# Kernel optimization log

Measured on AMD Instinct MI355X. Metric: run time of the kernel, lower is better.

The kernel has to match this reference:

```python
import jax, jax.numpy as jnp
from jax import lax
import numpy as np

B, C, H, W = 32, 128, 32, 32
ZDIM = 256
KH = KW = 3
NB_UNITS = C * C * KH * KW  # 147456
BN_EPS = 1e-6


def setup_inputs() -> dict:
    key = jax.random.key(0)
    ks = jax.random.split(key, 5)
    x = jax.random.normal(ks[0], (B, C, H, W), dtype=jnp.float32)
    z = jax.random.normal(ks[1], (B, ZDIM), dtype=jnp.float32)
    # glorot-uniform Dense kernel
    limit = np.sqrt(6.0 / (ZDIM + NB_UNITS)).astype(np.float32)
    dense_w = jax.random.uniform(ks[2], (ZDIM, NB_UNITS), dtype=jnp.float32,
                                 minval=-limit, maxval=limit)
    dense_b = jnp.zeros((NB_UNITS,), dtype=jnp.float32)
    # gamma initialized to +/- 0.02 (scale_for_weights)
    sign = jnp.where(jax.random.bernoulli(ks[3], 0.5, (NB_UNITS,)), 1.0, -1.0)
    gamma = (0.02 * sign).astype(jnp.float32)
    beta = jnp.zeros((NB_UNITS,), dtype=jnp.float32)
    b = jnp.zeros((C,), dtype=jnp.float32)  # deconv bias (zeros in original)
    return {"x": x, "z": z, "dense_w": dense_w, "dense_b": dense_b,
            "gamma": gamma, "beta": beta, "b": b}


def _per_sample_deconv(xi, wi):
    # xi: (C,H,W); wi: (C_in=stack, C_out=filter, KH, KW)
    # out[f,p,q] = sum_{s,u,v} xi[s, p+u-1, q+v-1] * wi[s,f,u,v]
    k = jnp.transpose(wi, (1, 0, 2, 3))  # OIHW: (f, s, u, v)
    y = lax.conv_general_dilated(xi[None], k, window_strides=(1, 1),
                                 padding=[(1, 1), (1, 1)],
                                 dimension_numbers=("NCHW", "OIHW", "NCHW"))
    return y[0]


def reference(x, z, dense_w, dense_b, gamma, beta, b):
    # hypernetwork: Dense(relu) -> BatchNorm(axis=1, batch stats) -> Reshape
    h = jax.nn.relu(z @ dense_w + dense_b)            # (B, NB_UNITS)
    mean = jnp.mean(h, axis=0)
    std = jnp.sqrt(jnp.var(h, axis=0))
    h = (h - mean) / (std + BN_EPS)
    h = gamma * h + beta
    Wk = h.reshape(B, C, C, KH, KW)                   # per-sample kernels (s,f,u,v)
    out = jax.vmap(_per_sample_deconv)(x, Wk)         # (B, C, H, W)
    out = out + b[None, :, None, None]
    return out + x                                    # residual add
```

## Files before the change

### kernel.cpp

```cpp
#include <hip/hip_runtime.h>

#define NB 147456
#define ZD 256
#define BSZ 32
#define CCH 128

typedef __attribute__((ext_vector_type(8))) short short8;
typedef __attribute__((ext_vector_type(16))) float floatx16;

__device__ __forceinline__ unsigned short f2bf(float f) {
    unsigned int u = __float_as_uint(f);
    return (unsigned short)((u + 0x7fffu + ((u >> 16) & 1u)) >> 16);
}
__device__ __forceinline__ unsigned pk(unsigned hi, unsigned lo) {
    return __builtin_amdgcn_perm(hi, lo, 0x07060302u);
}

__global__ __launch_bounds__(64, 4) void hyper_mfma(
    const float* __restrict__ z, const float* __restrict__ dw,
    const float* __restrict__ db, const float* __restrict__ gamma,
    const float* __restrict__ beta, unsigned short* __restrict__ wkn)
{
    int lane = threadIdx.x;
    int L = lane & 31;
    int klane = lane >> 5;
    int n0 = blockIdx.x * 64 + 2 * L;

    const float* zp  = z + L * 256 + klane * 8;
    const float* dwp = dw + (size_t)(klane * 8) * NB + n0;

    floatx16 acc[2];
#pragma unroll
    for (int t = 0; t < 2; t++)
#pragma unroll
        for (int r = 0; r < 16; r++) acc[t][r] = 0.f;

    float4 za[2], zb[2];
    unsigned ba[8][2], bb[8][2];
#define LOADZ(BUF, S)                                                         \
    { BUF[0] = *(const float4*)(zp + (S) * 16);                               \
      BUF[1] = *(const float4*)(zp + (S) * 16 + 4); }
#define LOADB(BUF, S)                                                         \
    _Pragma("unroll") for (int j = 0; j < 8; j++)                             \
        *(uint2*)&BUF[j][0] = *(const uint2*)(dwp + (size_t)((S) * 16 + j) * NB);
#define DOMFMA(ZBUF, BUF, S)                                                  \
    {                                                                         \
        uint4 au;                                                             \
        au.x = pk(__float_as_uint(ZBUF[0].y), __float_as_uint(ZBUF[0].x));    \
        au.y = pk(__float_as_uint(ZBUF[0].w), __float_as_uint(ZBUF[0].z));    \
        au.z = pk(__float_as_uint(ZBUF[1].y), __float_as_uint(ZBUF[1].x));    \
        au.w = pk(__float_as_uint(ZBUF[1].w), __float_as_uint(ZBUF[1].z));    \
        short8 af = *(short8*)&au;                                            \
        _Pragma("unroll") for (int t = 0; t < 2; t++) {                       \
            uint4 u;                                                          \
            u.x = pk(BUF[1][t], BUF[0][t]); u.y = pk(BUF[3][t], BUF[2][t]);   \
            u.z = pk(BUF[5][t], BUF[4][t]); u.w = pk(BUF[7][t], BUF[6][t]);   \
            acc[t] = __builtin_amdgcn_mfma_f32_32x32x16_bf16(                 \
                af, *(short8*)&u, acc[t], 0, 0, 0);                           \
        }                                                                     \
    }
    LOADZ(za, 0)
    LOADB(ba, 0)
#pragma unroll
    for (int s = 0; s < 16; s += 2) {
        LOADZ(zb, s + 1)
        LOADB(bb, s + 1)
        DOMFMA(za, ba, s)
        if (s + 2 < 16) { LOADZ(za, s + 2) LOADB(ba, s + 2) }
        DOMFMA(zb, bb, s + 1)
    }
#undef LOADZ
#undef LOADB
#undef DOMFMA

    float2 bias = *(const float2*)(db + n0);
    float2 gmm  = *(const float2*)(gamma + n0);
    float2 btt  = *(const float2*)(beta + n0);
    float bias_a[2] = { bias.x, bias.y };
    float gm_a[2]   = { gmm.x, gmm.y };
    float bt_a[2]   = { btt.x, btt.y };

    float sc_a[2], mn_a[2];
#pragma unroll
    for (int t = 0; t < 2; t++) {
        float sp = 0.f, qp = 0.f;
#pragma unroll
        for (int r = 0; r < 16; r++) {
            float v = fmaxf(acc[t][r] + bias_a[t], 0.f);
            acc[t][r] = v;
            sp += v; qp += v * v;
        }
        sp += __shfl_xor(sp, 32, 64);
        qp += __shfl_xor(qp, 32, 64);
        float mn = sp * (1.f / 32.f);
        float var = fmaxf(qp * (1.f / 32.f) - mn * mn, 0.f);
        mn_a[t] = mn;
        sc_a[t] = gm_a[t] / (sqrtf(var) + 1e-6f);
    }

#pragma unroll
    for (int r = 0; r < 16; r++) {
        int brow = (r & 3) + 8 * (r >> 2) + 4 * klane;
        float w0 = sc_a[0] * (acc[0][r] - mn_a[0]) + bt_a[0];
        float w1 = sc_a[1] * (acc[1][r] - mn_a[1]) + bt_a[1];
        unsigned o = (unsigned)f2bf(w0) | ((unsigned)f2bf(w1) << 16);
        *(unsigned*)&wkn[(size_t)brow * NB + n0] = o;
    }
}

__global__ __launch_bounds__(256) void repack_xt(
    const unsigned short* __restrict__ wkn, unsigned short* __restrict__ wkt,
    const float* __restrict__ x, unsigned short* __restrict__ xb16)
{
    __shared__ char lmem[16 * 580 * 4];
    int t = threadIdx.x;
    if (blockIdx.x < 256) {
        unsigned int* lt = (unsigned int*)lmem;
        int b = blockIdx.x >> 3;
        int s0 = (blockIdx.x & 7) * 16;
        const unsigned int* src = (const unsigned int*)wkn + ((size_t)b * NB >> 1) + (size_t)s0 * 576;
#pragma unroll
        for (int i = 0; i < 36; i++) {
            int idx = t + i * 256;
            int si = idx / 576;
            int j2 = idx - si * 576;
            lt[si * 580 + j2] = src[(size_t)si * 576 + j2];
        }
        __syncthreads();
        const unsigned short* ls = (const unsigned short*)lt;
#pragma unroll
        for (int i = 0; i < 9; i++) {
            int tau = t + i * 256;
            int f = tau & 127;
            int half = (tau >> 7) & 1;
            int uv = tau >> 8;
            int col = f * 9 + uv;
            unsigned short v[8];
#pragma unroll
            for (int ss = 0; ss < 8; ss++)
                v[ss] = ls[(half * 8 + ss) * 1160 + col];
            uint4 o;
            o.x = v[0] | ((unsigned)v[1] << 16);
            o.y = v[2] | ((unsigned)v[3] << 16);
            o.z = v[4] | ((unsigned)v[5] << 16);
            o.w = v[6] | ((unsigned)v[7] << 16);
            ((uint4*)wkt)[((((size_t)b * 9 + uv) * 16) + (s0 >> 3) + half) * 128 + f] = o;
        }
    } else {
        unsigned short* lx = (unsigned short*)lmem;
        int idx = blockIdx.x - 256;
        int p = idx & 31;
        int b = idx >> 5;
        const float* xp = x + (size_t)b * CCH * 1024 + p * 32;
#pragma unroll
        for (int i = 0; i < 16; i++) {
            int ii = t + i * 256;
            int s = ii >> 5;
            int q = ii & 31;
            lx[q * 130 + s] = f2bf(xp[(size_t)s * 1024 + q]);
        }
        __syncthreads();
#pragma unroll
        for (int i = 0; i < 2; i++) {
            int tau = t + i * 256;
            int q = tau & 31;
            int ch = tau >> 5;
            const unsigned short* r = &lx[q * 130 + ch * 8];
            uint4 o;
            o.x = r[0] | ((unsigned)r[1] << 16);
            o.y = r[2] | ((unsigned)r[3] << 16);
            o.z = r[4] | ((unsigned)r[5] << 16);
            o.w = r[6] | ((unsigned)r[7] << 16);
            ((uint4*)xb16)[(((size_t)b * 32 + p) * 16 + ch) * 32 + q] = o;
        }
    }
}

__global__ __launch_bounds__(256, 4) void conv_mfma(
    const float* __restrict__ x, const unsigned short* __restrict__ xb16,
    const unsigned short* __restrict__ wkt, const float* __restrict__ cb,
    float* __restrict__ out)
{
    __shared__ short8 lds8[3 * 16 * 34];
    int t = threadIdx.x;
    int w = blockIdx.x;
    int xcd = w & 7, slot = w >> 3;
    int b = (xcd << 2) | (slot & 3);
    int p0 = slot >> 2;
    int wid = t >> 6, lane = t & 63;
    int fbase = wid * 32;
    int qcol = lane & 31, klane = lane >> 5;

    if (t < 96) {
        int r = t >> 5;
        int ch = (t >> 1) & 15;
        int col = (t & 1) * 33;
        short8 zz = { 0, 0, 0, 0, 0, 0, 0, 0 };
        lds8[(r * 16 + ch) * 34 + col] = zz;
    }
    const uint4* xsrc = (const uint4*)xb16;
#pragma unroll
    for (int i = 0; i < 6; i++) {
        int tau = t + i * 256;
        int q = tau & 31;
        int ch = (tau >> 5) & 15;
        int r = tau >> 9;
        int prow = p0 - 1 + r;
        uint4 v = make_uint4(0, 0, 0, 0);
        if (prow >= 0 && prow < 32)
            v = xsrc[(((size_t)b * 32 + prow) * 16 + ch) * 32 + q];
        *(uint4*)&lds8[(r * 16 + ch) * 34 + q + 1] = v;
    }
    __syncthreads();

    floatx16 acc;
#pragma unroll
    for (int r = 0; r < 16; r++) acc[r] = 0.f;

    const short8* A8 = (const short8*)wkt + ((size_t)b * 9 << 11);
    short8 Abuf0[3], Abuf1[3];

#define LOAD3(BUF, ST)                                                        \
    {                                                                         \
        int v_ = (ST) >> 3, ks_ = (ST) & 7;                                   \
        int ko_ = ks_ * 2 + klane;                                            \
        _Pragma("unroll") for (int u_ = 0; u_ < 3; u_++)                      \
            BUF[u_] = A8[(((size_t)(u_ * 3 + v_) * 16 + ko_) << 7) + fbase + qcol]; \
    }
#define COMPUTE(BUF, ST)                                                      \
    {                                                                         \
        int v_ = (ST) >> 3, ks_ = (ST) & 7;                                   \
        int ko_ = ks_ * 2 + klane;                                            \
        short8 br[3];                                                         \
        _Pragma("unroll") for (int u_ = 0; u_ < 3; u_++)                      \
            br[u_] = lds8[(u_ * 16 + ko_) * 34 + qcol + v_];                  \
        _Pragma("unroll") for (int u_ = 0; u_ < 3; u_++)                      \
            acc = __builtin_amdgcn_mfma_f32_32x32x16_bf16(                    \
                BUF[u_], br[u_], acc, 0, 0, 0);                               \
    }

    LOAD3(Abuf0, 0)
    for (int st = 0; st < 24; st += 2) {
        LOAD3(Abuf1, st + 1)
        COMPUTE(Abuf0, st)
        if (st + 2 < 24) LOAD3(Abuf0, st + 2)
        COMPUTE(Abuf1, st + 1)
    }
#undef LOAD3
#undef COMPUTE

    const size_t xb = (size_t)b * CCH * 1024;
#pragma unroll
    for (int r = 0; r < 16; r++) {
        int fl = (r & 3) + 8 * (r >> 2) + 4 * klane;
        int f = fbase + fl;
        size_t idx = xb + (size_t)f * 1024 + p0 * 32 + qcol;
        out[idx] = acc[r] + x[idx] + cb[f];
    }
}

extern "C" void kernel_launch(void* const* d_in, const int* in_sizes, int n_in,
                              void* d_out, int out_size, void* d_ws, size_t ws_size,
                              hipStream_t stream) {
    const float* x     = (const float*)d_in[0];
    const float* z     = (const float*)d_in[1];
    const float* dw    = (const float*)d_in[2];
    const float* db    = (const float*)d_in[3];
    const float* gamma = (const float*)d_in[4];
    const float* beta  = (const float*)d_in[5];
    const float* cb    = (const float*)d_in[6];
    float* out = (float*)d_out;

    unsigned short* wkn  = (unsigned short*)d_ws;
    unsigned short* wkt  = (unsigned short*)((char*)d_ws + (size_t)BSZ * NB * 2);
    unsigned short* xb16 = (unsigned short*)((char*)d_ws + (size_t)BSZ * NB * 4);

    hyper_mfma<<<NB / 64, 64, 0, stream>>>(z, dw, db, gamma, beta, wkn);
    repack_xt<<<256 + 1024, 256, 0, stream>>>(wkn, wkt, x, xb16);
    conv_mfma<<<1024, 256, 0, stream>>>(x, xb16, wkt, cb, out);
}
```

Baseline: 262.0 us.

## Move x bf16 repack into hypernet kernel and triple-buffer conv weight loads

The x-to-bf16 transpose blocks move out of the weight repack kernel and are appended as extra 64-thread blocks of the hypernetwork kernel, so they run alongside the dense GEMM instead of in the repack launch. The repack kernel becomes weight-only. Separately, the conv kernel's A-operand prefetch goes from double to triple buffering with a fully unrolled loop, to hide more global-load latency. The extra blocks add LDS to every hyper_mfma block, and the third buffer adds registers, which may lower occupancy.

```diff
diff --git a/kernel.cpp b/kernel.cpp
--- a/kernel.cpp
+++ b/kernel.cpp
@@ -19,9 +19,41 @@
 __global__ __launch_bounds__(64, 4) void hyper_mfma(
     const float* __restrict__ z, const float* __restrict__ dw,
     const float* __restrict__ db, const float* __restrict__ gamma,
-    const float* __restrict__ beta, unsigned short* __restrict__ wkn)
+    const float* __restrict__ beta, unsigned short* __restrict__ wkn,
+    const float* __restrict__ x, unsigned short* __restrict__ xb16)
 {
+    __shared__ unsigned short lx[32 * 130];
     int lane = threadIdx.x;
+
+    if (blockIdx.x >= 2304) {
+        int idx = blockIdx.x - 2304;
+        int p = idx & 31;
+        int b = idx >> 5;
+        const float* xp = x + (size_t)b * CCH * 1024 + p * 32;
+#pragma unroll 8
+        for (int i = 0; i < 64; i++) {
+            int ii = lane + i * 64;
+            int s = ii >> 5;
+            int q = ii & 31;
+            lx[q * 130 + s] = f2bf(xp[(size_t)s * 1024 + q]);
+        }
+        __syncthreads();
+#pragma unroll
+        for (int i = 0; i < 8; i++) {
+            int tau = lane + i * 64;
+            int q = tau & 31;
+            int ch = tau >> 5;
+            const unsigned short* r = &lx[q * 130 + ch * 8];
+            uint4 o;
+            o.x = r[0] | ((unsigned)r[1] << 16);
+            o.y = r[2] | ((unsigned)r[3] << 16);
+            o.z = r[4] | ((unsigned)r[5] << 16);
+            o.w = r[6] | ((unsigned)r[7] << 16);
+            ((uint4*)xb16)[(((size_t)b * 32 + p) * 16 + ch) * 32 + q] = o;
+        }
+        return;
+    }
+
     int L = lane & 31;
     int klane = lane >> 5;
     int n0 = blockIdx.x * 64 + 2 * L;
@@ -108,71 +140,40 @@
     }
 }
 
-__global__ __launch_bounds__(256) void repack_xt(
-    const unsigned short* __restrict__ wkn, unsigned short* __restrict__ wkt,
-    const float* __restrict__ x, unsigned short* __restrict__ xb16)
+__global__ __launch_bounds__(256) void repack_w(
+    const unsigned short* __restrict__ wkn, unsigned short* __restrict__ wkt)
 {
-    __shared__ char lmem[16 * 580 * 4];
+    __shared__ unsigned int lt[16 * 580];
     int t = threadIdx.x;
-    if (blockIdx.x < 256) {
-        unsigned int* lt = (unsigned int*)lmem;
-        int b = blockIdx.x >> 3;
-        int s0 = (blockIdx.x & 7) * 16;
-        const unsigned int* src = (const unsigned int*)wkn + ((size_t)b * NB >> 1) + (size_t)s0 * 576;
-#pragma unroll
-        for (int i = 0; i < 36; i++) {
-            int idx = t + i * 256;
-            int si = idx / 576;
-            int j2 = idx - si * 576;
-            lt[si * 580 + j2] = src[(size_t)si * 576 + j2];
-        }
-        __syncthreads();
-        const unsigned short* ls = (const unsigned short*)lt;
-#pragma unroll
-        for (int i = 0; i < 9; i++) {
-            int tau = t + i * 256;
-            int f = tau & 127;
-            int half = (tau >> 7) & 1;
-            int uv = tau >> 8;
-            int col = f * 9 + uv;
-            unsigned short v[8];
-#pragma unroll
-            for (int ss = 0; ss < 8; ss++)
-                v[ss] = ls[(half * 8 + ss) * 1160 + col];
-            uint4 o;
-            o.x = v[0] | ((unsigned)v[1] << 16);
-            o.y = v[2] | ((unsigned)v[3] << 16);
-            o.z = v[4] | ((unsigned)v[5] << 16);
-            o.w = v[6] | ((unsigned)v[7] << 16);
-            ((uint4*)wkt)[((((size_t)b * 9 + uv) * 16) + (s0 >> 3) + half) * 128 + f] = o;
-        }
-    } else {
-        unsigned short* lx = (unsigned short*)lmem;
-        int idx = blockIdx.x - 256;
-        int p = idx & 31;
-        int b = idx >> 5;
-        const float* xp = x + (size_t)b * CCH * 1024 + p * 32;
-#pragma unroll
-        for (int i = 0; i < 16; i++) {
-            int ii = t + i * 256;
-            int s = ii >> 5;
-            int q = ii & 31;
-            lx[q * 130 + s] = f2bf(xp[(size_t)s * 1024 + q]);
-        }
-        __syncthreads();
-#pragma unroll
-        for (int i = 0; i < 2; i++) {
-            int tau = t + i * 256;
-            int q = tau & 31;
-            int ch = tau >> 5;
-            const unsigned short* r = &lx[q * 130 + ch * 8];
-            uint4 o;
-            o.x = r[0] | ((unsigned)r[1] << 16);
-            o.y = r[2] | ((unsigned)r[3] << 16);
-            o.z = r[4] | ((unsigned)r[5] << 16);
-            o.w = r[6] | ((unsigned)r[7] << 16);
-            ((uint4*)xb16)[(((size_t)b * 32 + p) * 16 + ch) * 32 + q] = o;
-        }
+    int b = blockIdx.x >> 3;
+    int s0 = (blockIdx.x & 7) * 16;
+    const unsigned int* src = (const unsigned int*)wkn + ((size_t)b * NB >> 1) + (size_t)s0 * 576;
+#pragma unroll
+    for (int i = 0; i < 36; i++) {
+        int idx = t + i * 256;
+        int si = idx / 576;
+        int j2 = idx - si * 576;
+        lt[si * 580 + j2] = src[(size_t)si * 576 + j2];
+    }
+    __syncthreads();
+    const unsigned short* ls = (const unsigned short*)lt;
+#pragma unroll
+    for (int i = 0; i < 9; i++) {
+        int tau = t + i * 256;
+        int f = tau & 127;
+        int half = (tau >> 7) & 1;
+        int uv = tau >> 8;
+        int col = f * 9 + uv;
+        unsigned short v[8];
+#pragma unroll
+        for (int ss = 0; ss < 8; ss++)
+            v[ss] = ls[(half * 8 + ss) * 1160 + col];
+        uint4 o;
+        o.x = v[0] | ((unsigned)v[1] << 16);
+        o.y = v[2] | ((unsigned)v[3] << 16);
+        o.z = v[4] | ((unsigned)v[5] << 16);
+        o.w = v[6] | ((unsigned)v[7] << 16);
+        ((uint4*)wkt)[((((size_t)b * 9 + uv) * 16) + (s0 >> 3) + half) * 128 + f] = o;
     }
 }
 
@@ -218,7 +219,7 @@
     for (int r = 0; r < 16; r++) acc[r] = 0.f;
 
     const short8* A8 = (const short8*)wkt + ((size_t)b * 9 << 11);
-    short8 Abuf0[3], Abuf1[3];
+    short8 A0[3], A1[3], A2[3];
 
 #define LOAD3(BUF, ST)                                                        \
     {                                                                         \
@@ -239,12 +240,16 @@
                 BUF[u_], br[u_], acc, 0, 0, 0);                               \
     }
 
-    LOAD3(Abuf0, 0)
-    for (int st = 0; st < 24; st += 2) {
-        LOAD3(Abuf1, st + 1)
-        COMPUTE(Abuf0, st)
-        if (st + 2 < 24) LOAD3(Abuf0, st + 2)
-        COMPUTE(Abuf1, st + 1)
+    LOAD3(A0, 0)
+    LOAD3(A1, 1)
+#pragma unroll
+    for (int st = 0; st < 24; st += 3) {
+        LOAD3(A2, st + 2)
+        COMPUTE(A0, st)
+        if (st + 3 < 24) LOAD3(A0, st + 3)
+        COMPUTE(A1, st + 1)
+        if (st + 4 < 24) LOAD3(A1, st + 4)
+        COMPUTE(A2, st + 2)
     }
 #undef LOAD3
 #undef COMPUTE
@@ -275,7 +280,7 @@
     unsigned short* wkt  = (unsigned short*)((char*)d_ws + (size_t)BSZ * NB * 2);
     unsigned short* xb16 = (unsigned short*)((char*)d_ws + (size_t)BSZ * NB * 4);
 
-    hyper_mfma<<<NB / 64, 64, 0, stream>>>(z, dw, db, gamma, beta, wkn);
-    repack_xt<<<256 + 1024, 256, 0, stream>>>(wkn, wkt, x, xb16);
+    hyper_mfma<<<2304 + 1024, 64, 0, stream>>>(z, dw, db, gamma, beta, wkn, x, xb16);
+    repack_w<<<256, 256, 0, stream>>>(wkn, wkt);
     conv_mfma<<<1024, 256, 0, stream>>>(x, xb16, wkt, cb, out);
 }
```

Result: no change. 266.2 us (+1.6%).
